# Performance work log

Hardware: AMD Instinct MI355X
Metric: run time of the kernel (lower is better)

Reference implementation:

```python
import jax, jax.numpy as jnp
import numpy as np

B, T, E, H = 4, 2048, 2048, 16
HD = E // H  # 128


def apply_rope(x, freqs):
    # x: (B, T, H, HD); freqs: (T, HD//2) rotation angles per position/pair
    cos = jnp.cos(freqs)[None, :, None, :]  # (1, T, 1, HD//2)
    sin = jnp.sin(freqs)[None, :, None, :]
    xr = x.reshape(*x.shape[:-1], HD // 2, 2)
    x1, x2 = xr[..., 0], xr[..., 1]
    out = jnp.stack([x1 * cos - x2 * sin, x1 * sin + x2 * cos], axis=-1)
    return out.reshape(x.shape)


def setup_inputs() -> dict:
    key = jax.random.key(0)
    k1, k2, k3, k4 = jax.random.split(key, 4)
    x = jax.random.normal(k1, (B, T, E), dtype=jnp.float32)
    freqs = jax.random.uniform(k2, (T, HD // 2), dtype=jnp.float32) * 6.28318
    w_qkv = jax.random.normal(k3, (3 * E, E), dtype=jnp.float32) * 0.02
    w_o = jax.random.normal(k4, (E, E), dtype=jnp.float32) * 0.02
    return {"x": x, "freqs": freqs, "w_qkv": w_qkv, "w_o": w_o}


def reference(x, freqs, w_qkv, w_o):
    b, t, e = x.shape
    qkv = x @ w_qkv.T                            # (B, T, 3E)
    qkv = qkv.reshape(b, t, 3, H, HD)
    q, k, v = qkv[:, :, 0], qkv[:, :, 1], qkv[:, :, 2]
    q = apply_rope(q, freqs)
    k = apply_rope(k, freqs)
    q = q.transpose(0, 2, 1, 3)                  # (B, H, T, HD)
    k = k.transpose(0, 2, 1, 3)
    v = v.transpose(0, 2, 1, 3)
    scale = 1.0 / np.sqrt(HD)
    scores = jnp.einsum('bhqd,bhkd->bhqk', q, k) * scale
    causal = jnp.tril(jnp.ones((t, t), dtype=bool))
    scores = jnp.where(causal[None, None], scores, jnp.finfo(scores.dtype).min)
    attn = jax.nn.softmax(scores, axis=-1)
    out = jnp.einsum('bhqk,bhkd->bhqd', attn, v)  # (B, H, T, HD)
    out = out.transpose(0, 2, 1, 3).reshape(b, t, e)
    return out @ w_o.T
```

## Files before the change

kernel.cpp:

```cpp
#include <hip/hip_runtime.h>
#include <type_traits>

#define DEV __device__ __forceinline__

typedef __attribute__((ext_vector_type(4))) float f32x4;
typedef __attribute__((ext_vector_type(8))) __bf16 bf16x8;
typedef __attribute__((ext_vector_type(8))) short s16x8;
typedef unsigned int u32;
typedef unsigned short u16;

DEV u16 f2bf(float f) {
  u32 u = __builtin_bit_cast(u32, f);
  u32 r = u + 0x7FFFu + ((u >> 16) & 1u);
  return (u16)(r >> 16);
}
DEV float bf2f(u16 h) {
  u32 u = ((u32)h) << 16;
  return __builtin_bit_cast(float, u);
}

template <typename A>
DEV auto mfma_sel(A a, A b, f32x4 c, int)
    -> decltype(__builtin_amdgcn_mfma_f32_16x16x32_bf16(a, b, c, 0, 0, 0)) {
  return __builtin_amdgcn_mfma_f32_16x16x32_bf16(a, b, c, 0, 0, 0);
}
template <typename A>
DEV f32x4 mfma_sel(A a, A b, f32x4 c, long) {
  using O = typename std::conditional<std::is_same<A, bf16x8>::value, s16x8, bf16x8>::type;
  return __builtin_amdgcn_mfma_f32_16x16x32_bf16(
      __builtin_bit_cast(O, a), __builtin_bit_cast(O, b), c, 0, 0, 0);
}
DEV f32x4 MFMA16(bf16x8 a, bf16x8 b, f32x4 c) { return mfma_sel(a, b, c, 0); }

DEV void gload_lds16(const void* g, void* l) {
  __builtin_amdgcn_global_load_lds(
      (__attribute__((address_space(1))) void*)(g),
      (__attribute__((address_space(3))) void*)(l), 16, 0, 0);
}

__global__ __launch_bounds__(256) void prologue(const float* __restrict__ x,
                                                const float* __restrict__ wq,
                                                const float* __restrict__ wo,
                                                const float* __restrict__ freqs,
                                                u16* __restrict__ x_bf,
                                                u16* __restrict__ wq_bf,
                                                u16* __restrict__ wo_bf,
                                                float2* __restrict__ cst) {
  const int b = blockIdx.x;
  auto cvt_seg = [&](const float* in, u16* out, int i, int n4, int stride) {
    for (; i < n4; i += stride) {
      const float4 v = ((const float4*)in)[i];
      ushort4 o;
      o.x = f2bf(v.x); o.y = f2bf(v.y); o.z = f2bf(v.z); o.w = f2bf(v.w);
      ((ushort4*)out)[i] = o;
    }
  };
  if (b < 2048) {
    cvt_seg(x, x_bf, b * 256 + threadIdx.x, 8192 * 2048 / 4, 2048 * 256);
  } else if (b < 2048 + 768) {
    cvt_seg(wq, wq_bf, (b - 2048) * 256 + threadIdx.x, 6144 * 2048 / 4, 768 * 256);
  } else if (b < 2048 + 768 + 256) {
    cvt_seg(wo, wo_bf, (b - 2816) * 256 + threadIdx.x, 2048 * 2048 / 4, 256 * 256);
  } else {
    const int i = (b - 3072) * 256 + threadIdx.x;
    if (i < 131072) {
      float f = freqs[i];
      cst[i] = make_float2(cosf(f), sinf(f));
    }
  }
}

template <int MODE>
__global__ __launch_bounds__(512, 2) void gemm_bt(const u16* __restrict__ A,
                                                  const u16* __restrict__ Bm,
                                                  void* __restrict__ Cp,
                                                  u16* __restrict__ q_r,
                                                  u16* __restrict__ k_r,
                                                  u16* __restrict__ v_t,
                                                  const float2* __restrict__ cst,
                                                  const int M, const int N, const int K) {
  __shared__ __align__(16) u16 SH[65536];
  const int tid = threadIdx.x;
  const int wid = tid >> 6;
  const int lane = tid & 63;
  const int lrow = lane & 15;
  const int lgrp = lane >> 4;

  const int gx = gridDim.x;
  const int nwg = gx * gridDim.y;
  int id = blockIdx.y * gx + blockIdx.x;
  const int cpx = nwg >> 3;
  id = (id & 7) * cpx + (id >> 3);
  const int row0 = (id / gx) * 256;
  const int col0 = (id % gx) * 256;

  const int wm = (wid >> 2) * 128;
  const int wn = (wid & 3) * 64;

  f32x4 acc[8][4] = {};

  const int sj0 = wid * 2;
  const int srow = lane >> 2;
  const int sc = lane & 3;

#define STAGE_HALF(SLOT, T, II)                                                   \
  do {                                                                            \
    const int j_ = sj0 + (II);                                                    \
    const int row_ = j_ * 16 + srow;                                              \
    const int ch_ = sc ^ ((row_ >> 1) & 3);                                       \
    const int k0_ = (T) * 32;                                                     \
    gload_lds16(A + (size_t)(row0 + row_) * K + k0_ + ch_ * 8,                    \
                (char*)SH + (SLOT) * 16384 + j_ * 1024);                          \
    gload_lds16(Bm + (size_t)(col0 + row_) * K + k0_ + ch_ * 8,                   \
                (char*)SH + 65536 + (SLOT) * 16384 + j_ * 1024);                  \
  } while (0)

#define READS_B(SLOT)                                                             \
  _Pragma("unroll") for (int fn = 0; fn < 4; ++fn) {                              \
    const int brow_ = wn + fn * 16 + lrow;                                        \
    bfr[fn] = *(const bf16x8*)((const char*)SH + 65536 + (SLOT) * 16384 +         \
                               brow_ * 64 + ((lgrp ^ ((brow_ >> 1) & 3)) << 4));  \
  }

#define READS_A(SLOT, QUAD)                                                       \
  _Pragma("unroll") for (int i_ = 0; i_ < 4; ++i_) {                              \
    const int arow_ = wm + ((QUAD) * 4 + i_) * 16 + lrow;                         \
    af[i_] = *(const bf16x8*)((const char*)SH + (SLOT) * 16384 +                  \
                              arow_ * 64 + ((lgrp ^ ((arow_ >> 1) & 3)) << 4));   \
  }

#define MFMA_QUAD(QUAD)                                                           \
  __builtin_amdgcn_s_setprio(1);                                                  \
  _Pragma("unroll") for (int fm = 0; fm < 4; ++fm) {                              \
    _Pragma("unroll") for (int fn = 0; fn < 4; ++fn)                              \
      acc[(QUAD) * 4 + fm][fn] = MFMA16(af[fm], bfr[fn], acc[(QUAD) * 4 + fm][fn]); \
  }                                                                               \
  __builtin_amdgcn_s_setprio(0);

  const int nk = K >> 5;
  STAGE_HALF(0, 0, 0); STAGE_HALF(0, 0, 1);
  STAGE_HALF(1, 1, 0); STAGE_HALF(1, 1, 1);
  STAGE_HALF(2, 2, 0); STAGE_HALF(2, 2, 1);
  __builtin_amdgcn_sched_barrier(0);
  asm volatile("s_waitcnt vmcnt(8)" ::: "memory");
  __builtin_amdgcn_s_barrier();

  bf16x8 bfr[4], af[4];
  for (int t = 0; t < nk - 2; ++t) {
    const int slot = t & 3;
    const int ns = (t + 3) & 3;
    const bool dostage = (t + 3) < nk;
    READS_B(slot)
    READS_A(slot, 0)
    if (dostage) STAGE_HALF(ns, t + 3, 0);
    __builtin_amdgcn_sched_barrier(0);
    __builtin_amdgcn_s_barrier();
    MFMA_QUAD(0)
    __builtin_amdgcn_sched_barrier(0);
    __builtin_amdgcn_s_barrier();
    READS_A(slot, 1)
    if (dostage) STAGE_HALF(ns, t + 3, 1);
    __builtin_amdgcn_sched_barrier(0);
    __builtin_amdgcn_s_barrier();
    MFMA_QUAD(1)
    __builtin_amdgcn_sched_barrier(0);
    asm volatile("s_waitcnt vmcnt(8)" ::: "memory");
    __builtin_amdgcn_s_barrier();
  }
  {
    const int slot = (nk - 2) & 3;
    READS_B(slot) READS_A(slot, 0)
    __builtin_amdgcn_sched_barrier(0);
    __builtin_amdgcn_s_barrier();
    MFMA_QUAD(0)
    __builtin_amdgcn_s_barrier();
    READS_A(slot, 1)
    __builtin_amdgcn_sched_barrier(0);
    __builtin_amdgcn_s_barrier();
    MFMA_QUAD(1)
    __builtin_amdgcn_sched_barrier(0);
    asm volatile("s_waitcnt vmcnt(0)" ::: "memory");
    __builtin_amdgcn_s_barrier();
  }
  {
    const int slot = (nk - 1) & 3;
    READS_B(slot) READS_A(slot, 0)
    __builtin_amdgcn_sched_barrier(0);
    __builtin_amdgcn_s_barrier();
    MFMA_QUAD(0)
    __builtin_amdgcn_s_barrier();
    READS_A(slot, 1)
    MFMA_QUAD(1)
  }

  if constexpr (MODE == 0) {
    #pragma unroll
    for (int fm = 0; fm < 8; ++fm) {
      #pragma unroll
      for (int r = 0; r < 4; ++r) {
        const size_t rb = (size_t)(row0 + wm + fm * 16 + lgrp * 4 + r) * N + col0 + wn + lrow;
        #pragma unroll
        for (int fn = 0; fn < 4; ++fn)
          ((float*)Cp)[rb + fn * 16] = acc[fm][fn][r];
      }
    }
  } else {
    const int which = col0 >> 11;
    if (which < 2) {
      const int colw = (col0 & 2047) + wn;
      const int h = colw >> 7;
      const int d0 = colw & 127;
      u16* const dst0 = (which == 0) ? q_r : k_r;
      const float wscale = (which == 0) ? (0.08838834765f * 1.44269504089f) : 1.0f;
      #pragma unroll
      for (int fm = 0; fm < 8; ++fm) {
        #pragma unroll
        for (int r = 0; r < 4; ++r) {
          const int grow = row0 + wm + fm * 16 + lgrp * 4 + r;
          const int bb = grow >> 11, tt = grow & 2047;
          u16* const drow = dst0 + (((size_t)(bb * 16 + h) * 2048 + tt) << 7);
          #pragma unroll
          for (int fn = 0; fn < 4; ++fn) {
            const float v = acc[fm][fn][r];
            const float p = __shfl_xor(v, 1);
            const int d = d0 + fn * 16 + lrow;
            const float2 cs = cst[tt * 64 + (d >> 1)];
            const float o = ((lrow & 1) ? (p * cs.y + v * cs.x) : (v * cs.x - p * cs.y)) * wscale;
            drow[d] = f2bf(o);
          }
        }
      }
    } else {
      const int hbase = (col0 - 4096) >> 7;
      const int bb = row0 >> 11;
      const int tloc0 = row0 & 2047;
      const int hd = tid >> 1, half = tid & 1;
      const int hh = hd >> 7, dd = hd & 127;
      u16* const dstb = v_t + ((size_t)(bb * 16 + hbase + hh) * 128 + dd) * 2048;
      #pragma unroll
      for (int c = 0; c < 2; ++c) {
        __builtin_amdgcn_s_barrier();
        if ((wm >> 7) == c) {
          #pragma unroll
          for (int fm = 0; fm < 8; ++fm) {
            #pragma unroll
            for (int r = 0; r < 4; ++r) {
              const int rl = fm * 16 + lgrp * 4 + r;
              #pragma unroll
              for (int fn = 0; fn < 4; ++fn)
                SH[rl * 260 + wn + fn * 16 + lrow] = f2bf(acc[fm][fn][r]);
            }
          }
        }
        __builtin_amdgcn_s_barrier();
        u16* dst = dstb + tloc0 + c * 128 + half * 64;
        #pragma unroll
        for (int seg = 0; seg < 8; ++seg) {
          const int tb = (half * 64 + seg * 8) * 260 + hd;
          u32 w0 = (u32)SH[tb]        | ((u32)SH[tb + 260] << 16);
          u32 w1 = (u32)SH[tb + 520]  | ((u32)SH[tb + 780] << 16);
          u32 w2 = (u32)SH[tb + 1040] | ((u32)SH[tb + 1300] << 16);
          u32 w3 = (u32)SH[tb + 1560] | ((u32)SH[tb + 1820] << 16);
          uint4 w = make_uint4(w0, w1, w2, w3);
          *(uint4*)(dst + seg * 8) = w;
        }
      }
    }
  }
#undef STAGE_HALF
#undef READS_B
#undef READS_A
#undef MFMA_QUAD
}

__global__ __launch_bounds__(512, 2) void attn_fwd(const u16* __restrict__ Qp,
                                                   const u16* __restrict__ Kp,
                                                   const u16* __restrict__ Vp,
                                                   u16* __restrict__ Op) {
  constexpr int T = 2048;
  __shared__ __align__(16) u16 Kl[3][64 * 128];
  __shared__ __align__(16) u16 Vl[3][128 * 64];
  __shared__ __align__(16) u16 Pl[8 * 2048];

  const int tid = threadIdx.x;
  const int wid = tid >> 6;
  const int lane = tid & 63;
  const int lrow = lane & 15;
  const int lgrp = lane >> 4;

  const int lin = blockIdx.y * 4 + blockIdx.x;
  const int qa = lin >> 6;
  const int bh = ((lin & 7) << 3) | ((lin >> 3) & 7);

  const u16* Qb = Qp + (size_t)bh * T * 128;
  const u16* Kb = Kp + (size_t)bh * T * 128;
  const u16* Vb = Vp + (size_t)bh * 128 * T;

  const float DTH = 12.0f;
  const int s0 = (lane & 48) + ((lane & 48) >> 2);
  char* Pw = (char*)Pl + wid * 4096;
  const int ob = bh >> 4, oh = bh & 15;

  auto stage = [&](int buf, int kv0) {
    #pragma unroll
    for (int ii = 0; ii < 2; ++ii) {
      const int i = wid * 2 + ii;
      {
        const int rr = i * 4 + (lane >> 4);
        const int cs = (lane & 15) ^ (rr & 7);
        gload_lds16(Kb + (size_t)(kv0 + rr) * 128 + cs * 8, (char*)&Kl[buf][0] + i * 1024);
      }
      {
        const int rr = i * 8 + (lane >> 3);
        const int cs = (lane & 7) ^ (rr & 7);
        gload_lds16(Vb + (size_t)rr * T + kv0 + cs * 8, (char*)&Vl[buf][0] + i * 1024);
      }
    }
  };

  auto process = [&](const int qi) {
    const int q0 = qi * 256;
    const int wq0 = q0 + wid * 32;

    bf16x8 qf[2][4];
    #pragma unroll
    for (int qg = 0; qg < 2; ++qg) {
      const int qrow = wq0 + qg * 16 + lrow;
      #pragma unroll
      for (int db = 0; db < 4; ++db)
        qf[qg][db] = *(const bf16x8*)(Qb + (size_t)qrow * 128 + db * 32 + lgrp * 8);
    }

    f32x4 o[2][8] = {};
    float m[2] = {-3e38f, -3e38f};
    float l[2] = {0.f, 0.f};

    const int nkv = 4 * qi + 4;
    stage(0, 0);
    stage(1, 64);
    int csl = 0;
    for (int j = 0; j < nkv; ++j) {
      if (j < nkv - 1) asm volatile("s_waitcnt vmcnt(4)" ::: "memory");
      else             asm volatile("s_waitcnt vmcnt(0)" ::: "memory");
      __builtin_amdgcn_s_barrier();
      if (j + 2 < nkv) {
        int ss = csl + 2; if (ss >= 3) ss -= 3;
        stage(ss, (j + 2) * 64);
      }
      const int kv0 = j * 64;

      if (kv0 <= wq0 + 31) {
        f32x4 s[2][4] = {};
        __builtin_amdgcn_s_setprio(1);
        #pragma unroll
        for (int t4 = 0; t4 < 4; ++t4) {
          const int krow = t4 * 16 + lrow;
          #pragma unroll
          for (int db = 0; db < 4; ++db) {
            const int ch = (db * 4 + lgrp) ^ (krow & 7);
            bf16x8 kf = *(const bf16x8*)((const char*)&Kl[csl][0] + krow * 256 + ch * 16);
            s[0][t4] = MFMA16(kf, qf[0][db], s[0][t4]);
            s[1][t4] = MFMA16(kf, qf[1][db], s[1][t4]);
          }
        }
        __builtin_amdgcn_s_setprio(0);

        if (kv0 + 63 > wq0) {
          #pragma unroll
          for (int qg = 0; qg < 2; ++qg) {
            const int lim = wq0 + qg * 16 + lrow - kv0 - lgrp * 4;
            #pragma unroll
            for (int t4 = 0; t4 < 4; ++t4) {
              #pragma unroll
              for (int r = 0; r < 4; ++r)
                if (t4 * 16 + r > lim) s[qg][t4][r] = -3e38f;
            }
          }
        }

        float pmax[2];
        #pragma unroll
        for (int qg = 0; qg < 2; ++qg) {
          float pm = fmaxf(fmaxf(s[qg][0][0], s[qg][0][1]), fmaxf(s[qg][0][2], s[qg][0][3]));
          #pragma unroll
          for (int t4 = 1; t4 < 4; ++t4)
            pm = fmaxf(pm, fmaxf(fmaxf(s[qg][t4][0], s[qg][t4][1]),
                                 fmaxf(s[qg][t4][2], s[qg][t4][3])));
          pm = fmaxf(pm, __shfl_xor(pm, 16));
          pm = fmaxf(pm, __shfl_xor(pm, 32));
          pmax[qg] = pm;
        }

        float alpha[2] = {1.f, 1.f};
        const float dmax = fmaxf(pmax[0] - m[0], pmax[1] - m[1]);
        if (__any(dmax > DTH)) {
          #pragma unroll
          for (int qg = 0; qg < 2; ++qg) {
            const float mn = fmaxf(m[qg], pmax[qg]);
            alpha[qg] = exp2f(m[qg] - mn);
            m[qg] = mn;
          }
          #pragma unroll
          for (int qg = 0; qg < 2; ++qg) {
            #pragma unroll
            for (int r = 0; r < 4; ++r) {
              const float a4 = __shfl(alpha[qg], s0 + r);
              #pragma unroll
              for (int db = 0; db < 8; ++db)
                o[qg][db][r] *= a4;
            }
          }
        }

        float psum[2] = {0.f, 0.f};
        #pragma unroll
        for (int qg = 0; qg < 2; ++qg) {
          #pragma unroll
          for (int t4 = 0; t4 < 4; ++t4) {
            #pragma unroll
            for (int r = 0; r < 4; ++r) {
              const float p = exp2f(s[qg][t4][r] - m[qg]);
              s[qg][t4][r] = p;
              psum[qg] += p;
            }
          }
          psum[qg] += __shfl_xor(psum[qg], 16);
          psum[qg] += __shfl_xor(psum[qg], 32);
          l[qg] = l[qg] * alpha[qg] + psum[qg];
        }

        #pragma unroll
        for (int qg = 0; qg < 2; ++qg) {
          #pragma unroll
          for (int t4 = 0; t4 < 4; ++t4) {
            uint2 w;
            w.x = (u32)f2bf(s[qg][t4][0]) | ((u32)f2bf(s[qg][t4][1]) << 16);
            w.y = (u32)f2bf(s[qg][t4][2]) | ((u32)f2bf(s[qg][t4][3]) << 16);
            const int off = lrow * 128 + (((t4 * 2 + (lgrp >> 1)) ^ (lrow & 7)) << 4) + (lgrp & 1) * 8;
            *(uint2*)(Pw + qg * 2048 + off) = w;
          }
        }
        asm volatile("s_waitcnt lgkmcnt(0)" ::: "memory");
        __builtin_amdgcn_sched_barrier(0);

        bf16x8 pa[2][2];
        #pragma unroll
        for (int qg = 0; qg < 2; ++qg) {
          #pragma unroll
          for (int kb = 0; kb < 2; ++kb)
            pa[qg][kb] = *(const bf16x8*)(Pw + qg * 2048 + lrow * 128 +
                                          (((kb * 4 + lgrp) ^ (lrow & 7)) << 4));
        }
        __builtin_amdgcn_s_setprio(1);
        #pragma unroll
        for (int db = 0; db < 8; ++db) {
          const int vrow = db * 16 + lrow;
          #pragma unroll
          for (int kb = 0; kb < 2; ++kb) {
            const int vch = (kb * 4 + lgrp) ^ (vrow & 7);
            bf16x8 vf = *(const bf16x8*)((const char*)&Vl[csl][0] + vrow * 128 + vch * 16);
            o[0][db] = MFMA16(pa[0][kb], vf, o[0][db]);
            o[1][db] = MFMA16(pa[1][kb], vf, o[1][db]);
          }
        }
        __builtin_amdgcn_s_setprio(0);
      }
      csl = (csl == 2) ? 0 : csl + 1;
    }

    #pragma unroll
    for (int qg = 0; qg < 2; ++qg) {
      const float inv = 1.f / l[qg];
      float inv4[4];
      #pragma unroll
      for (int r = 0; r < 4; ++r) inv4[r] = __shfl(inv, s0 + r);
      #pragma unroll
      for (int db = 0; db < 8; ++db) {
        #pragma unroll
        for (int r = 0; r < 4; ++r) {
          const int qrow = wq0 + qg * 16 + lgrp * 4 + r;
          Op[((size_t)ob * T + qrow) * 2048 + oh * 128 + db * 16 + lrow] =
              f2bf(o[qg][db][r] * inv4[r]);
        }
      }
    }
  };

  process(7 - qa);
  __syncthreads();
  process(qa);
}

extern "C" void kernel_launch(void* const* d_in, const int* in_sizes, int n_in,
                              void* d_out, int out_size, void* d_ws, size_t ws_size,
                              hipStream_t stream) {
  const float* x = (const float*)d_in[0];
  const float* freqs = (const float*)d_in[1];
  const float* w_qkv = (const float*)d_in[2];
  const float* w_o = (const float*)d_in[3];

  constexpr int B = 4, T = 2048, E = 2048, H = 16;
  constexpr size_t M = (size_t)B * T;
  constexpr int N3 = 3 * E;

  char* ws = (char*)d_ws;
  size_t off = 0;
  auto alloc = [&](size_t bytes) {
    void* p = ws + off;
    off += (bytes + 255) & ~(size_t)255;
    return p;
  };
  u16* wqkv_bf = (u16*)alloc((size_t)N3 * E * 2);
  u16* wo_bf   = (u16*)alloc((size_t)E * E * 2);
  u16* x_bf    = (u16*)alloc(M * E * 2);
  u16* q_r     = (u16*)alloc(M * E * 2);
  u16* k_r     = (u16*)alloc(M * E * 2);
  u16* vt      = (u16*)alloc(M * E * 2);
  u16* attn_o  = (u16*)alloc(M * E * 2);
  float2* cst  = (float2*)alloc((size_t)T * 64 * 8);

  prologue<<<3584, 256, 0, stream>>>(x, w_qkv, w_o, freqs, x_bf, wqkv_bf, wo_bf, cst);

  gemm_bt<2><<<dim3(N3 / 256, (int)(M / 256)), 512, 0, stream>>>(
      x_bf, wqkv_bf, nullptr, q_r, k_r, vt, cst, (int)M, N3, E);
  attn_fwd<<<dim3(4, B * H), 512, 0, stream>>>(q_r, k_r, vt, attn_o);
  gemm_bt<0><<<dim3(E / 256, (int)(M / 256)), 512, 0, stream>>>(
      attn_o, wo_bf, d_out, nullptr, nullptr, nullptr, nullptr, (int)M, E, E);
}
```

Baseline: 432.8 us.

## Software-pipeline QK of next KV tile with softmax and PV of current

Splits the attention inner loop into a QK^T phase and a softmax-plus-PV phase. The loop is unrolled by two with ping-pong score registers, so the QK MFMAs for tile j+1 are issued before the softmax and PV work of tile j. The K/V shared-memory ring grows from three to four slots, prefetching three tiles ahead, so loads stay ahead of the deeper pipeline. The goal is to hide the exp/reduction latency behind matrix-core work. The cost is a second set of score registers and more LDS, which now totals 160KB per block, so occupancy and spilling are risks.

```diff
diff --git a/kernel.cpp b/kernel.cpp
--- a/kernel.cpp
+++ b/kernel.cpp
@@ -278,8 +278,8 @@
                                                    const u16* __restrict__ Vp,
                                                    u16* __restrict__ Op) {
   constexpr int T = 2048;
-  __shared__ __align__(16) u16 Kl[3][64 * 128];
-  __shared__ __align__(16) u16 Vl[3][128 * 64];
+  __shared__ __align__(16) u16 Kl[4][64 * 128];
+  __shared__ __align__(16) u16 Vl[4][128 * 64];
   __shared__ __align__(16) u16 Pl[8 * 2048];
 
   const int tid = threadIdx.x;
@@ -335,137 +335,158 @@
     float m[2] = {-3e38f, -3e38f};
     float l[2] = {0.f, 0.f};
 
-    const int nkv = 4 * qi + 4;
-    stage(0, 0);
-    stage(1, 64);
-    int csl = 0;
-    for (int j = 0; j < nkv; ++j) {
-      if (j < nkv - 1) asm volatile("s_waitcnt vmcnt(4)" ::: "memory");
-      else             asm volatile("s_waitcnt vmcnt(0)" ::: "memory");
-      __builtin_amdgcn_s_barrier();
-      if (j + 2 < nkv) {
-        int ss = csl + 2; if (ss >= 3) ss -= 3;
-        stage(ss, (j + 2) * 64);
-      }
+    auto qk = [&](int j, f32x4 (&s)[2][4]) {
       const int kv0 = j * 64;
-
-      if (kv0 <= wq0 + 31) {
-        f32x4 s[2][4] = {};
-        __builtin_amdgcn_s_setprio(1);
-        #pragma unroll
-        for (int t4 = 0; t4 < 4; ++t4) {
-          const int krow = t4 * 16 + lrow;
-          #pragma unroll
-          for (int db = 0; db < 4; ++db) {
-            const int ch = (db * 4 + lgrp) ^ (krow & 7);
-            bf16x8 kf = *(const bf16x8*)((const char*)&Kl[csl][0] + krow * 256 + ch * 16);
-            s[0][t4] = MFMA16(kf, qf[0][db], s[0][t4]);
-            s[1][t4] = MFMA16(kf, qf[1][db], s[1][t4]);
-          }
-        }
-        __builtin_amdgcn_s_setprio(0);
-
-        if (kv0 + 63 > wq0) {
-          #pragma unroll
-          for (int qg = 0; qg < 2; ++qg) {
-            const int lim = wq0 + qg * 16 + lrow - kv0 - lgrp * 4;
-            #pragma unroll
-            for (int t4 = 0; t4 < 4; ++t4) {
-              #pragma unroll
-              for (int r = 0; r < 4; ++r)
-                if (t4 * 16 + r > lim) s[qg][t4][r] = -3e38f;
-            }
-          }
-        }
-
-        float pmax[2];
+      if (kv0 > wq0 + 31) return;
+      const int csl = j & 3;
+      #pragma unroll
+      for (int qg = 0; qg < 2; ++qg)
+        #pragma unroll
+        for (int t4 = 0; t4 < 4; ++t4) s[qg][t4] = f32x4{0.f, 0.f, 0.f, 0.f};
+      __builtin_amdgcn_s_setprio(1);
+      #pragma unroll
+      for (int t4 = 0; t4 < 4; ++t4) {
+        const int krow = t4 * 16 + lrow;
+        #pragma unroll
+        for (int db = 0; db < 4; ++db) {
+          const int ch = (db * 4 + lgrp) ^ (krow & 7);
+          bf16x8 kf = *(const bf16x8*)((const char*)&Kl[csl][0] + krow * 256 + ch * 16);
+          s[0][t4] = MFMA16(kf, qf[0][db], s[0][t4]);
+          s[1][t4] = MFMA16(kf, qf[1][db], s[1][t4]);
+        }
+      }
+      __builtin_amdgcn_s_setprio(0);
+    };
+
+    auto smpv = [&](int j, f32x4 (&s)[2][4]) {
+      const int kv0 = j * 64;
+      if (kv0 > wq0 + 31) return;
+      const int csl = j & 3;
+
+      if (kv0 + 63 > wq0) {
         #pragma unroll
         for (int qg = 0; qg < 2; ++qg) {
-          float pm = fmaxf(fmaxf(s[qg][0][0], s[qg][0][1]), fmaxf(s[qg][0][2], s[qg][0][3]));
-          #pragma unroll
-          for (int t4 = 1; t4 < 4; ++t4)
-            pm = fmaxf(pm, fmaxf(fmaxf(s[qg][t4][0], s[qg][t4][1]),
-                                 fmaxf(s[qg][t4][2], s[qg][t4][3])));
-          pm = fmaxf(pm, __shfl_xor(pm, 16));
-          pm = fmaxf(pm, __shfl_xor(pm, 32));
-          pmax[qg] = pm;
-        }
-
-        float alpha[2] = {1.f, 1.f};
-        const float dmax = fmaxf(pmax[0] - m[0], pmax[1] - m[1]);
-        if (__any(dmax > DTH)) {
-          #pragma unroll
-          for (int qg = 0; qg < 2; ++qg) {
-            const float mn = fmaxf(m[qg], pmax[qg]);
-            alpha[qg] = exp2f(m[qg] - mn);
-            m[qg] = mn;
-          }
-          #pragma unroll
-          for (int qg = 0; qg < 2; ++qg) {
-            #pragma unroll
-            for (int r = 0; r < 4; ++r) {
-              const float a4 = __shfl(alpha[qg], s0 + r);
-              #pragma unroll
-              for (int db = 0; db < 8; ++db)
-                o[qg][db][r] *= a4;
-            }
-          }
-        }
-
-        float psum[2] = {0.f, 0.f};
-        #pragma unroll
-        for (int qg = 0; qg < 2; ++qg) {
+          const int lim = wq0 + qg * 16 + lrow - kv0 - lgrp * 4;
           #pragma unroll
           for (int t4 = 0; t4 < 4; ++t4) {
             #pragma unroll
-            for (int r = 0; r < 4; ++r) {
-              const float p = exp2f(s[qg][t4][r] - m[qg]);
-              s[qg][t4][r] = p;
-              psum[qg] += p;
-            }
+            for (int r = 0; r < 4; ++r)
+              if (t4 * 16 + r > lim) s[qg][t4][r] = -3e38f;
           }
-          psum[qg] += __shfl_xor(psum[qg], 16);
-          psum[qg] += __shfl_xor(psum[qg], 32);
-          l[qg] = l[qg] * alpha[qg] + psum[qg];
-        }
-
+        }
+      }
+
+      float pmax[2];
+      #pragma unroll
+      for (int qg = 0; qg < 2; ++qg) {
+        float pm = fmaxf(fmaxf(s[qg][0][0], s[qg][0][1]), fmaxf(s[qg][0][2], s[qg][0][3]));
+        #pragma unroll
+        for (int t4 = 1; t4 < 4; ++t4)
+          pm = fmaxf(pm, fmaxf(fmaxf(s[qg][t4][0], s[qg][t4][1]),
+                               fmaxf(s[qg][t4][2], s[qg][t4][3])));
+        pm = fmaxf(pm, __shfl_xor(pm, 16));
+        pm = fmaxf(pm, __shfl_xor(pm, 32));
+        pmax[qg] = pm;
+      }
+
+      float alpha[2] = {1.f, 1.f};
+      const float dmax = fmaxf(pmax[0] - m[0], pmax[1] - m[1]);
+      if (__any(dmax > DTH)) {
+        #pragma unroll
+        for (int qg = 0; qg < 2; ++qg) {
+          const float mn = fmaxf(m[qg], pmax[qg]);
+          alpha[qg] = exp2f(m[qg] - mn);
+          m[qg] = mn;
+        }
         #pragma unroll
         for (int qg = 0; qg < 2; ++qg) {
           #pragma unroll
-          for (int t4 = 0; t4 < 4; ++t4) {
-            uint2 w;
-            w.x = (u32)f2bf(s[qg][t4][0]) | ((u32)f2bf(s[qg][t4][1]) << 16);
-            w.y = (u32)f2bf(s[qg][t4][2]) | ((u32)f2bf(s[qg][t4][3]) << 16);
-            const int off = lrow * 128 + (((t4 * 2 + (lgrp >> 1)) ^ (lrow & 7)) << 4) + (lgrp & 1) * 8;
-            *(uint2*)(Pw + qg * 2048 + off) = w;
+          for (int r = 0; r < 4; ++r) {
+            const float a4 = __shfl(alpha[qg], s0 + r);
+            #pragma unroll
+            for (int db = 0; db < 8; ++db)
+              o[qg][db][r] *= a4;
           }
         }
-        asm volatile("s_waitcnt lgkmcnt(0)" ::: "memory");
-        __builtin_amdgcn_sched_barrier(0);
-
-        bf16x8 pa[2][2];
-        #pragma unroll
-        for (int qg = 0; qg < 2; ++qg) {
+      }
+
+      float psum[2] = {0.f, 0.f};
+      #pragma unroll
+      for (int qg = 0; qg < 2; ++qg) {
+        #pragma unroll
+        for (int t4 = 0; t4 < 4; ++t4) {
           #pragma unroll
-          for (int kb = 0; kb < 2; ++kb)
-            pa[qg][kb] = *(const bf16x8*)(Pw + qg * 2048 + lrow * 128 +
-                                          (((kb * 4 + lgrp) ^ (lrow & 7)) << 4));
-        }
-        __builtin_amdgcn_s_setprio(1);
-        #pragma unroll
-        for (int db = 0; db < 8; ++db) {
-          const int vrow = db * 16 + lrow;
-          #pragma unroll
-          for (int kb = 0; kb < 2; ++kb) {
-            const int vch = (kb * 4 + lgrp) ^ (vrow & 7);
-            bf16x8 vf = *(const bf16x8*)((const char*)&Vl[csl][0] + vrow * 128 + vch * 16);
-            o[0][db] = MFMA16(pa[0][kb], vf, o[0][db]);
-            o[1][db] = MFMA16(pa[1][kb], vf, o[1][db]);
+          for (int r = 0; r < 4; ++r) {
+            const float p = exp2f(s[qg][t4][r] - m[qg]);
+            s[qg][t4][r] = p;
+            psum[qg] += p;
           }
         }
-        __builtin_amdgcn_s_setprio(0);
-      }
-      csl = (csl == 2) ? 0 : csl + 1;
+        psum[qg] += __shfl_xor(psum[qg], 16);
+        psum[qg] += __shfl_xor(psum[qg], 32);
+        l[qg] = l[qg] * alpha[qg] + psum[qg];
+      }
+
+      #pragma unroll
+      for (int qg = 0; qg < 2; ++qg) {
+        #pragma unroll
+        for (int t4 = 0; t4 < 4; ++t4) {
+          uint2 w;
+          w.x = (u32)f2bf(s[qg][t4][0]) | ((u32)f2bf(s[qg][t4][1]) << 16);
+          w.y = (u32)f2bf(s[qg][t4][2]) | ((u32)f2bf(s[qg][t4][3]) << 16);
+          const int off = lrow * 128 + (((t4 * 2 + (lgrp >> 1)) ^ (lrow & 7)) << 4) + (lgrp & 1) * 8;
+          *(uint2*)(Pw + qg * 2048 + off) = w;
+        }
+      }
+      asm volatile("s_waitcnt lgkmcnt(0)" ::: "memory");
+      __builtin_amdgcn_sched_barrier(0);
+
+      bf16x8 pa[2][2];
+      #pragma unroll
+      for (int qg = 0; qg < 2; ++qg) {
+        #pragma unroll
+        for (int kb = 0; kb < 2; ++kb)
+          pa[qg][kb] = *(const bf16x8*)(Pw + qg * 2048 + lrow * 128 +
+                                        (((kb * 4 + lgrp) ^ (lrow & 7)) << 4));
+      }
+      __builtin_amdgcn_s_setprio(1);
+      #pragma unroll
+      for (int db = 0; db < 8; ++db) {
+        const int vrow = db * 16 + lrow;
+        #pragma unroll
+        for (int kb = 0; kb < 2; ++kb) {
+          const int vch = (kb * 4 + lgrp) ^ (vrow & 7);
+          bf16x8 vf = *(const bf16x8*)((const char*)&Vl[csl][0] + vrow * 128 + vch * 16);
+          o[0][db] = MFMA16(pa[0][kb], vf, o[0][db]);
+          o[1][db] = MFMA16(pa[1][kb], vf, o[1][db]);
+        }
+      }
+      __builtin_amdgcn_s_setprio(0);
+    };
+
+    const int nkv = 4 * qi + 4;
+    f32x4 sA[2][4], sB[2][4];
+
+    stage(0, 0);
+    stage(1, 64);
+    stage(2, 128);
+    asm volatile("s_waitcnt vmcnt(4)" ::: "memory");
+    __builtin_amdgcn_s_barrier();
+    qk(0, sA);
+
+    for (int j = 0; j < nkv; j += 2) {
+      if (j + 3 < nkv) stage((j + 3) & 3, (j + 3) * 64);
+      if (j + 1 < nkv) qk(j + 1, sB);
+      smpv(j, sA);
+      if (j + 3 < nkv) asm volatile("s_waitcnt vmcnt(4)" ::: "memory");
+      else             asm volatile("s_waitcnt vmcnt(0)" ::: "memory");
+      __builtin_amdgcn_s_barrier();
+      if (j + 4 < nkv) stage((j + 4) & 3, (j + 4) * 64);
+      if (j + 2 < nkv) qk(j + 2, sA);
+      smpv(j + 1, sB);
+      if (j + 4 < nkv) asm volatile("s_waitcnt vmcnt(4)" ::: "memory");
+      else             asm volatile("s_waitcnt vmcnt(0)" ::: "memory");
+      __builtin_amdgcn_s_barrier();
     }
 
     #pragma unroll
```

New measurement: 438.3 us. About the same (+1.3%).
